# Kernel tuning notes

Hardware: AMD Instinct MI355X
Metric: run time of the kernel (lower is better)

The kernel has to match this reference:

```python
import jax, jax.numpy as jnp
import numpy as np

N = 50000
E = 800000
F = 64
HID = 64
HEADS = 4
NTYPES = 3


def layer_norm(x, g, b, eps=1e-5):
    mu = x.mean(-1, keepdims=True)
    var = ((x - mu) ** 2).mean(-1, keepdims=True)
    return (x - mu) * jax.lax.rsqrt(var + eps) * g + b


def gat_conv(x, src, dst, n, W, att_src, att_dst, bias, concat):
    # PyG GATConv: per-head linear transform, additive attention, segment softmax over dst.
    H, C = att_src.shape
    xp = (x @ W).reshape(n, H, C)                       # [N,H,C]
    a_s = (xp * att_src).sum(-1)                         # [N,H]
    a_d = (xp * att_dst).sum(-1)                         # [N,H]
    e = jax.nn.leaky_relu(a_s[src] + a_d[dst], 0.2)      # [Etot,H]
    m = jax.ops.segment_max(e, dst, num_segments=n)      # stable softmax per target
    ex = jnp.exp(e - m[dst])
    denom = jax.ops.segment_sum(ex, dst, num_segments=n)
    alpha = ex / (denom[dst] + 1e-16)                    # [Etot,H]
    msg = xp[src] * alpha[:, :, None]                    # [Etot,H,C]
    out = jax.ops.segment_sum(msg, dst, num_segments=n)  # [N,H,C]
    out = out.reshape(n, H * C) if concat else out.mean(1)
    return out + bias


def setup_inputs() -> dict:
    key = jax.random.key(0)
    ks = jax.random.split(key, 12)
    f32 = jnp.float32
    return {
        'node_features': jax.random.normal(ks[0], (N, F), f32),
        'node_types': jax.random.randint(ks[1], (N,), 0, NTYPES),
        'edge_index': jax.random.randint(ks[2], (2, E), 0, N),
        'type_emb': jax.random.normal(ks[3], (NTYPES, HID), f32) * 0.02,
        'proj_W': jax.random.normal(ks[4], (F, HID), f32) / np.sqrt(F).astype(np.float32),
        'proj_b': jnp.zeros((HID,), f32),
        'W0': jax.random.normal(ks[5], (HID, HEADS * HID), f32) / np.sqrt(HID).astype(np.float32),
        'att_src0': jax.random.normal(ks[6], (HEADS, HID), f32) * 0.1,
        'att_dst0': jax.random.normal(ks[7], (HEADS, HID), f32) * 0.1,
        'bias0': jnp.zeros((HEADS * HID,), f32),
        'ln0_g': jnp.ones((HEADS * HID,), f32),
        'ln0_b': jnp.zeros((HEADS * HID,), f32),
        'W1': jax.random.normal(ks[8], (HEADS * HID, HEADS * HID), f32) / np.sqrt(HEADS * HID).astype(np.float32),
        'att_src1': jax.random.normal(ks[9], (HEADS, HID), f32) * 0.1,
        'att_dst1': jax.random.normal(ks[10], (HEADS, HID), f32) * 0.1,
        'bias1': jnp.zeros((HID,), f32),
        'ln1_g': jnp.ones((HID,), f32),
        'ln1_b': jnp.zeros((HID,), f32),
    }


def reference(node_features, node_types, edge_index, type_emb, proj_W, proj_b,
              W0, att_src0, att_dst0, bias0, ln0_g, ln0_b,
              W1, att_src1, att_dst1, bias1, ln1_g, ln1_b):
    n = node_features.shape[0]
    loop = jnp.arange(n)
    src = jnp.concatenate([edge_index[0], loop])  # add_self_loops=True (PyG default)
    dst = jnp.concatenate([edge_index[1], loop])
    # input projection + node-type embedding
    x = node_features @ proj_W + proj_b + type_emb[node_types]
    # layer 0: concat heads -> [N, HEADS*HID]
    h = gat_conv(x, src, dst, n, W0, att_src0, att_dst0, bias0, True)
    h = jax.nn.relu(layer_norm(h, ln0_g, ln0_b))  # dropout is identity in eval
    # layer 1: mean over heads -> [N, HID]; residual skipped (shape mismatch 256 vs 64)
    h2 = gat_conv(h, src, dst, n, W1, att_src1, att_dst1, bias1, False)
    h2 = jax.nn.relu(layer_norm(h2, ln1_g, ln1_b))
    return h2
```

## Files before the change

### kernel.cpp

```cpp
#include <hip/hip_runtime.h>
#include <hip/hip_bf16.h>
#include <hip/hip_fp16.h>

typedef unsigned short u16;
typedef unsigned int u32;
typedef short s16x8 __attribute__((ext_vector_type(8)));
typedef float f32x4 __attribute__((ext_vector_type(4)));

__device__ __forceinline__ float bf2f(u16 u) {
  return __uint_as_float(((u32)u) << 16);
}

__device__ __forceinline__ u16 f2b(float f) {
  __hip_bfloat16 h = __float2bfloat16(f);
  return *(u16*)&h;
}

__device__ __forceinline__ u32 packbf(float lo, float hi) {
  return (u32)f2b(lo) | ((u32)f2b(hi) << 16);
}

__device__ __forceinline__ bool sniff_bf16(const void* ones) {
  u32 w = *(const u32*)ones;
  return (w >> 16) == (w & 0xFFFFu);
}

__device__ __forceinline__ float ldf(const void* p, size_t i, bool bf) {
  return bf ? bf2f(((const u16*)p)[i]) : ((const float*)p)[i];
}

__device__ __forceinline__ float rdlane_f(float v, int e) {
  return __uint_as_float((u32)__builtin_amdgcn_readlane((int)__float_as_uint(v), e));
}

__global__ __launch_bounds__(256) void deg_count_k(const int* __restrict__ ei, int E, int N,
                                                   int* __restrict__ deg) {
  int i = blockIdx.x * 256 + threadIdx.x;
  if (i >= E + N) return;
  int d = (i < E) ? ei[E + i] : (i - E);
  atomicAdd(deg + d, 1);
}

__global__ __launch_bounds__(256) void scan_local_k(const int* __restrict__ deg,
                                                    int* __restrict__ off,
                                                    int* __restrict__ bsum, int N) {
  __shared__ int ps[256];
  int t = threadIdx.x;
  int i = blockIdx.x * 256 + t;
  int v = (i < N) ? deg[i] : 0;
  ps[t] = v;
  __syncthreads();
#pragma unroll
  for (int o = 1; o < 256; o <<= 1) {
    int u = (t >= o) ? ps[t - o] : 0;
    __syncthreads();
    ps[t] += u;
    __syncthreads();
  }
  if (i < N) off[i] = ps[t] - v;
  if (t == 255) bsum[blockIdx.x] = ps[255];
}

__global__ __launch_bounds__(256) void scan_add2_k(int* __restrict__ off,
                                                   const int* __restrict__ bsum,
                                                   int* __restrict__ cur,
                                                   int N, int Etot, int nb) {
  __shared__ int red[256];
  int t = threadIdx.x;
  int b = blockIdx.x;
  red[t] = (t < nb && t < b) ? bsum[t] : 0;
  __syncthreads();
#pragma unroll
  for (int o = 128; o > 0; o >>= 1) {
    if (t < o) red[t] += red[t + o];
    __syncthreads();
  }
  int pre = red[0];
  int i = b * 256 + t;
  if (i == 0) off[N] = Etot;
  if (i >= N) return;
  int o2 = off[i] + pre;
  off[i] = o2;
  cur[i] = o2;
}

__global__ __launch_bounds__(256) void scatter_k(const int* __restrict__ ei, int E, int N,
                                                 int* __restrict__ cur, int* __restrict__ csr) {
  int i = blockIdx.x * 256 + threadIdx.x;
  if (i >= E + N) return;
  int s, d;
  if (i < E) { s = ei[i]; d = ei[E + i]; } else { s = i - E; d = s; }
  int p = atomicAdd(cur + d, 1);
  csr[p] = s;
}

__global__ __launch_bounds__(256) void prep_k(
    const void* __restrict__ W0, const void* __restrict__ W1,
    const void* __restrict__ pW, const void* __restrict__ atts,
    const void* __restrict__ attd, const void* __restrict__ pb,
    const void* __restrict__ temb, const void* __restrict__ ones,
    u16* __restrict__ Wp0, u16* __restrict__ Wp1, u16* __restrict__ Wpp,
    u16* __restrict__ Wpe, float* __restrict__ ca) {
  bool bf = sniff_bf16(ones);
  int b = blockIdx.x;
  int t = threadIdx.x;
  if (b < 320) {
    const void* W = (b < 64) ? W0 : W1;
    u16* Wp = (b < 64) ? Wp0 : Wp1;
    int i = (b < 64 ? b : b - 64) * 256 + t;
    int j = i & 7;
    int q = (i >> 3) & 3;
    int c = (i >> 5) & 255;
    int kc = i >> 13;
    int k = kc * 32 + q * 8 + j;
    Wp[i] = f2b(ldf(W, (size_t)k * 256 + c, bf));
  } else if (b < 336) {
    int i = (b - 320) * 256 + t;
    int j = i & 7;
    int q = (i >> 3) & 3;
    int c = (i >> 5) & 63;
    int kc = i >> 11;
    int k = kc * 32 + q * 8 + j;
    Wpp[i] = f2b(ldf(pW, (size_t)k * 64 + c, bf));
  } else {
    __shared__ float va[256], vd[256];
    int h = t >> 6, k = t & 63;
    {
      float s = 0.f, d = 0.f;
      for (int c = 0; c < 64; c++) {
        float w = ldf(W0, (size_t)k * 256 + h * 64 + c, bf);
        s += w * ldf(atts, h * 64 + c, bf);
        d += w * ldf(attd, h * 64 + c, bf);
      }
      va[t] = s;
      vd[t] = d;
    }
    __syncthreads();
    {
      int i = k;
      float wa = 0.f, wd = 0.f;
      for (int kk = 0; kk < 64; kk++) {
        float wv = ldf(pW, (size_t)i * 64 + kk, bf);
        wa += wv * va[h * 64 + kk];
        wd += wv * vd[h * 64 + kk];
      }
      int kc = i >> 5, q = (i >> 3) & 3, j = i & 7;
      Wpe[((kc * 16 + h) * 4 + q) * 8 + j] = f2b(wa);
      Wpe[((kc * 16 + 4 + h) * 4 + q) * 8 + j] = f2b(wd);
    }
    Wpe[256 + t] = 0;
    Wpe[768 + t] = 0;
    if (t < 12) {
      int ty = t >> 2, hh = t & 3;
      float sa = 0.f, sd = 0.f;
      for (int kk = 0; kk < 64; kk++) {
        float bv = ldf(pb, kk, bf) + ldf(temb, ty * 64 + kk, bf);
        sa += bv * va[hh * 64 + kk];
        sd += bv * vd[hh * 64 + kk];
      }
      ca[t] = sa;
      ca[12 + t] = sd;
    }
  }
}

__global__ __launch_bounds__(256) void proj2_k(
    const void* __restrict__ nf, const int* __restrict__ ntype,
    const u16* __restrict__ Wpp, const u16* __restrict__ Wpe,
    const void* __restrict__ pbias, const void* __restrict__ temb,
    const float* __restrict__ ca, const void* __restrict__ ones,
    u16* __restrict__ x, float* __restrict__ aS, float* __restrict__ aD, int N) {
  bool bf = sniff_bf16(ones);
  int t = threadIdx.x;
  int wave = t >> 6, lane = t & 63;
  int r = lane & 15, q = lane >> 4;
  int row0 = blockIdx.x * 16;
  int arow = row0 + r;
  if (arow >= N) arow = N - 1;
  f32x4 xacc = {0.f, 0.f, 0.f, 0.f};
  f32x4 eacc = {0.f, 0.f, 0.f, 0.f};
#pragma unroll
  for (int kc = 0; kc < 2; kc++) {
    s16x8 a;
    if (bf) {
      a = *(const s16x8*)((const u16*)nf + (size_t)arow * 64 + kc * 32 + q * 8);
    } else {
      const float* fp = (const float*)nf + (size_t)arow * 64 + kc * 32 + q * 8;
#pragma unroll
      for (int j = 0; j < 8; j++) a[j] = (short)f2b(fp[j]);
    }
    {
      int c = wave * 16 + r;
      s16x8 b = *(const s16x8*)(Wpp + (((size_t)kc * 64 + c) * 4 + q) * 8);
      xacc = __builtin_amdgcn_mfma_f32_16x16x32_bf16(a, b, xacc, 0, 0, 0);
    }
    if (wave == 3) {
      s16x8 b = *(const s16x8*)(Wpe + (((size_t)kc * 16 + r) * 4 + q) * 8);
      eacc = __builtin_amdgcn_mfma_f32_16x16x32_bf16(a, b, eacc, 0, 0, 0);
    }
  }
#pragma unroll
  for (int rg = 0; rg < 4; rg++) {
    int row = row0 + q * 4 + rg;
    if (row >= N) continue;
    int col = wave * 16 + r;
    int ty = ntype[row];
    float v = xacc[rg] + ldf(pbias, col, bf) + ldf(temb, ty * 64 + col, bf);
    x[(size_t)row * 64 + col] = f2b(v);
    if (wave == 3 && r < 8) {
      if (r < 4) aS[(size_t)row * 4 + r] = eacc[rg] + ca[ty * 4 + r];
      else       aD[(size_t)row * 4 + (r - 4)] = eacc[rg] + ca[12 + ty * 4 + (r - 4)];
    }
  }
}

__global__ __launch_bounds__(256) void agg0_k(
    const int* __restrict__ off, const int* __restrict__ csr,
    const float* __restrict__ aS, const float* __restrict__ aD,
    const u16* __restrict__ x, u16* __restrict__ Ag, int N) {
  int n = blockIdx.x * 4 + (threadIdx.x >> 6);
  int lane = threadIdx.x & 63;
  if (n >= N) return;
  int start = off[n], end = off[n + 1];
  float4 ad4 = *(const float4*)(aD + (size_t)n * 4);
  float ad[4] = {ad4.x, ad4.y, ad4.z, ad4.w};
  float den[4] = {0.f, 0.f, 0.f, 0.f};
  float acc[4] = {0.f, 0.f, 0.f, 0.f};
  const u16* xl = x + lane;

  for (int cs = start; cs < end; cs += 64) {
    int cnt = end - cs; if (cnt > 64) cnt = 64;
    int s = 0;
    float ex[4] = {0.f, 0.f, 0.f, 0.f};
    if (lane < cnt) {
      s = csr[cs + lane];
      float4 as4 = *(const float4*)(aS + (size_t)s * 4);
      float av[4] = {as4.x, as4.y, as4.z, as4.w};
#pragma unroll
      for (int h = 0; h < 4; h++) {
        float v = av[h] + ad[h];
        v = (v > 0.f ? v : 0.2f * v) - 3.0f;
        ex[h] = __expf(v);
        den[h] += ex[h];
      }
    }
#pragma unroll 8
    for (int e = 0; e < cnt; e++) {
      int se = __builtin_amdgcn_readlane(s, e);
      float w0 = rdlane_f(ex[0], e);
      float w1 = rdlane_f(ex[1], e);
      float w2 = rdlane_f(ex[2], e);
      float w3 = rdlane_f(ex[3], e);
      float xv = bf2f(xl[(size_t)se * 64]);
      acc[0] += w0 * xv;
      acc[1] += w1 * xv;
      acc[2] += w2 * xv;
      acc[3] += w3 * xv;
    }
  }
#pragma unroll
  for (int h = 0; h < 4; h++) {
#pragma unroll
    for (int o = 32; o > 0; o >>= 1) den[h] += __shfl_xor(den[h], o, 64);
    acc[h] /= (den[h] + 1e-16f);
  }
#pragma unroll
  for (int h = 0; h < 4; h++) Ag[(size_t)n * 256 + h * 64 + lane] = f2b(acc[h]);
}

__global__ __launch_bounds__(256) void l0g1_k(
    const u16* __restrict__ Ag, const u16* __restrict__ Wp0,
    const void* __restrict__ bias0, const void* __restrict__ g0,
    const void* __restrict__ be0, const u16* __restrict__ Wp1,
    const void* __restrict__ atts, const void* __restrict__ attd,
    const void* __restrict__ ones,
    u16* __restrict__ C, float* __restrict__ aS, float* __restrict__ aD, int N) {
  bool bf = sniff_bf16(ones);
  __shared__ u16 hs[16][264];
  __shared__ float sm_s[4][16], sm_q[4][16];
  int t = threadIdx.x;
  int wave = t >> 6, lane = t & 63;
  int r = lane & 15, q = lane >> 4;
  int row0 = blockIdx.x * 16;
  int arow = row0 + r;
  if (arow >= N) arow = N - 1;
  {
    const u16* ap = Ag + (size_t)arow * 256 + wave * 64 + q * 8;
    f32x4 acc[4] = {{0.f, 0.f, 0.f, 0.f}, {0.f, 0.f, 0.f, 0.f},
                    {0.f, 0.f, 0.f, 0.f}, {0.f, 0.f, 0.f, 0.f}};
#pragma unroll
    for (int kc = 0; kc < 2; kc++) {
      s16x8 a = *(const s16x8*)(ap + kc * 32);
#pragma unroll
      for (int ct = 0; ct < 4; ct++) {
        int c = wave * 64 + ct * 16 + r;
        s16x8 b = *(const s16x8*)(Wp0 + (((size_t)kc * 256 + c) * 4 + q) * 8);
        acc[ct] = __builtin_amdgcn_mfma_f32_16x16x32_bf16(a, b, acc[ct], 0, 0, 0);
      }
    }
    float yv[4][4];
    float s_p[4] = {0.f, 0.f, 0.f, 0.f};
    float q_p[4] = {0.f, 0.f, 0.f, 0.f};
#pragma unroll
    for (int ct = 0; ct < 4; ct++) {
      float bc = ldf(bias0, wave * 64 + ct * 16 + r, bf);
#pragma unroll
      for (int rg = 0; rg < 4; rg++) {
        float y = acc[ct][rg] + bc;
        yv[ct][rg] = y;
        s_p[rg] += y;
        q_p[rg] += y * y;
      }
    }
#pragma unroll
    for (int o = 1; o < 16; o <<= 1) {
#pragma unroll
      for (int rg = 0; rg < 4; rg++) {
        s_p[rg] += __shfl_xor(s_p[rg], o, 64);
        q_p[rg] += __shfl_xor(q_p[rg], o, 64);
      }
    }
    if (r == 0) {
#pragma unroll
      for (int rg = 0; rg < 4; rg++) {
        sm_s[wave][q * 4 + rg] = s_p[rg];
        sm_q[wave][q * 4 + rg] = q_p[rg];
      }
    }
    __syncthreads();
#pragma unroll
    for (int rg = 0; rg < 4; rg++) {
      int lr = q * 4 + rg;
      float mu = (sm_s[0][lr] + sm_s[1][lr] + sm_s[2][lr] + sm_s[3][lr]) * (1.f / 256.f);
      float vq = (sm_q[0][lr] + sm_q[1][lr] + sm_q[2][lr] + sm_q[3][lr]) * (1.f / 256.f) - mu * mu;
      float inv = rsqrtf(vq + 1e-5f);
#pragma unroll
      for (int ct = 0; ct < 4; ct++) {
        int c = wave * 64 + ct * 16 + r;
        float o_ = (yv[ct][rg] - mu) * inv * ldf(g0, c, bf) + ldf(be0, c, bf);
        hs[lr][c] = f2b(fmaxf(o_, 0.f));
      }
    }
  }
  __syncthreads();
  int colw = wave * 64;
  f32x4 acc[4] = {{0.f, 0.f, 0.f, 0.f}, {0.f, 0.f, 0.f, 0.f},
                  {0.f, 0.f, 0.f, 0.f}, {0.f, 0.f, 0.f, 0.f}};
#pragma unroll
  for (int kc = 0; kc < 8; kc++) {
    s16x8 a = *(const s16x8*)&hs[r][kc * 32 + q * 8];
#pragma unroll
    for (int ct = 0; ct < 4; ct++) {
      int c = colw + ct * 16 + r;
      s16x8 b = *(const s16x8*)(Wp1 + (((size_t)kc * 256 + c) * 4 + q) * 8);
      acc[ct] = __builtin_amdgcn_mfma_f32_16x16x32_bf16(a, b, acc[ct], 0, 0, 0);
    }
  }
#pragma unroll
  for (int ct = 0; ct < 4; ct++) {
#pragma unroll
    for (int rg = 0; rg < 4; rg++) {
      int row = row0 + q * 4 + rg;
      if (row < N) C[(size_t)row * 256 + colw + ct * 16 + r] = f2b(acc[ct][rg]);
    }
  }
  float sp[4] = {0.f, 0.f, 0.f, 0.f};
  float dp[4] = {0.f, 0.f, 0.f, 0.f};
#pragma unroll
  for (int ct = 0; ct < 4; ct++) {
    int c = colw + ct * 16 + r;
    float av = ldf(atts, c, bf);
    float dv = ldf(attd, c, bf);
#pragma unroll
    for (int rg = 0; rg < 4; rg++) {
      sp[rg] += acc[ct][rg] * av;
      dp[rg] += acc[ct][rg] * dv;
    }
  }
#pragma unroll
  for (int o = 1; o < 16; o <<= 1) {
#pragma unroll
    for (int rg = 0; rg < 4; rg++) {
      sp[rg] += __shfl_xor(sp[rg], o, 64);
      dp[rg] += __shfl_xor(dp[rg], o, 64);
    }
  }
  if (r == 0) {
#pragma unroll
    for (int rg = 0; rg < 4; rg++) {
      int row = row0 + q * 4 + rg;
      if (row < N) {
        aS[(size_t)row * 4 + wave] = sp[rg];
        aD[(size_t)row * 4 + wave] = dp[rg];
      }
    }
  }
}

__global__ __launch_bounds__(256) void agg1_k(
    const int* __restrict__ off, const int* __restrict__ csr,
    const float* __restrict__ aS, const float* __restrict__ aD,
    const u16* __restrict__ xp,
    const void* __restrict__ bias, const void* __restrict__ g,
    const void* __restrict__ b, void* __restrict__ out, int N) {
  bool bf = sniff_bf16(g);
  int n = blockIdx.x * 4 + (threadIdx.x >> 6);
  int lane = threadIdx.x & 63;
  if (n >= N) return;
  int start = off[n], end = off[n + 1];
  bool hiSel = (lane & 32) != 0;
  float4 ad4 = *(const float4*)(aD + (size_t)n * 4);
  float ad[4] = {ad4.x, ad4.y, ad4.z, ad4.w};
  float den[4] = {0.f, 0.f, 0.f, 0.f};
  float acc[4] = {0.f, 0.f, 0.f, 0.f};
  const u32* xp32 = (const u32*)xp;

  for (int cs = start; cs < end; cs += 64) {
    int cnt = end - cs; if (cnt > 64) cnt = 64;
    int s = 0;
    float ex[4] = {0.f, 0.f, 0.f, 0.f};
    if (lane < cnt) {
      s = csr[cs + lane];
      float4 as4 = *(const float4*)(aS + (size_t)s * 4);
      float av[4] = {as4.x, as4.y, as4.z, as4.w};
#pragma unroll
      for (int h = 0; h < 4; h++) {
        float v = av[h] + ad[h];
        v = (v > 0.f ? v : 0.2f * v) - 3.0f;
        ex[h] = __expf(v);
        den[h] += ex[h];
      }
    }
#pragma unroll 8
    for (int e = 0; e < cnt; e++) {
      int se = __builtin_amdgcn_readlane(s, e);
      float w0 = rdlane_f(ex[0], e);
      float w1 = rdlane_f(ex[1], e);
      float w2 = rdlane_f(ex[2], e);
      float w3 = rdlane_f(ex[3], e);
      float wA = hiSel ? w1 : w0;
      float wB = hiSel ? w3 : w2;
      const u32* xr = xp32 + (size_t)se * 128 + lane;
      u32 dA = xr[0];
      u32 dB = xr[64];
      acc[0] += wA * __uint_as_float(dA << 16);
      acc[1] += wA * __uint_as_float(dA & 0xffff0000u);
      acc[2] += wB * __uint_as_float(dB << 16);
      acc[3] += wB * __uint_as_float(dB & 0xffff0000u);
    }
  }
#pragma unroll
  for (int h = 0; h < 4; h++) {
#pragma unroll
    for (int o = 32; o > 0; o >>= 1) den[h] += __shfl_xor(den[h], o, 64);
  }
  {
    float dA = (hiSel ? den[1] : den[0]) + 1e-16f;
    float dB = (hiSel ? den[3] : den[2]) + 1e-16f;
    acc[0] /= dA; acc[1] /= dA;
    acc[2] /= dB; acc[3] /= dB;
  }
  float p0 = acc[0] + acc[2];
  float p1 = acc[1] + acc[3];
  p0 += __shfl_xor(p0, 32, 64);
  p1 += __shfl_xor(p1, 32, 64);
  int c = 2 * (lane & 31);
  float z0 = 0.25f * p0 + ldf(bias, c, bf);
  float z1 = 0.25f * p1 + ldf(bias, c + 1, bf);
  float sum = z0 + z1;
#pragma unroll
  for (int o = 32; o > 0; o >>= 1) sum += __shfl_xor(sum, o, 64);
  float mu = sum * (1.f / 128.f);
  float d0 = z0 - mu, d1 = z1 - mu;
  float sq = d0 * d0 + d1 * d1;
#pragma unroll
  for (int o = 32; o > 0; o >>= 1) sq += __shfl_xor(sq, o, 64);
  float inv = rsqrtf(sq * (1.f / 128.f) + 1e-5f);
  float y0 = fmaxf(d0 * inv * ldf(g, c, bf) + ldf(b, c, bf), 0.f);
  float y1 = fmaxf(d1 * inv * ldf(g, c + 1, bf) + ldf(b, c + 1, bf), 0.f);
  if (lane < 32) {
    if (bf) {
      ((u32*)out)[(size_t)n * 32 + lane] = packbf(y0, y1);
    } else {
      ((float2*)out)[(size_t)n * 32 + lane] = make_float2(y0, y1);
    }
  }
}

extern "C" void kernel_launch(void* const* d_in, const int* in_sizes, int n_in,
                              void* d_out, int out_size, void* d_ws, size_t ws_size,
                              hipStream_t stream) {
  const void* nf   = d_in[0];
  const int* ntyp  = (const int*)d_in[1];
  const int* ei    = (const int*)d_in[2];
  const void* temb = d_in[3];
  const void* pW   = d_in[4];
  const void* pb   = d_in[5];
  const void* W0   = d_in[6];
  const void* as0  = d_in[7];
  const void* ad0  = d_in[8];
  const void* b0   = d_in[9];
  const void* g0   = d_in[10];
  const void* be0  = d_in[11];
  const void* W1   = d_in[12];
  const void* as1  = d_in[13];
  const void* ad1  = d_in[14];
  const void* b1   = d_in[15];
  const void* g1   = d_in[16];
  const void* be1  = d_in[17];

  int N = in_sizes[0] / 64;
  int E = in_sizes[2] / 2;
  int Etot = E + N;

  u16* Wp0 = (u16*)d_ws;
  u16* Wp1 = Wp0 + 64 * 256;
  u16* Wpp = Wp1 + 256 * 256;
  u16* Wpe = Wpp + 64 * 64;
  u16* xb  = Wpe + 1024;
  u16* Ag  = xb + (size_t)N * 64;
  u16* A   = Ag + (size_t)N * 256;
  float* aS0b = (float*)(A + (size_t)N * 256);
  float* aD0b = aS0b + (size_t)N * 4;
  float* aS1b = aD0b + (size_t)N * 4;
  float* aD1b = aS1b + (size_t)N * 4;
  float* ca = aD1b + (size_t)N * 4;
  int* deg  = (int*)(ca + 32);
  int* off  = deg + N;
  int* csr  = off + N + 1;
  int* bsum = csr + Etot;

  dim3 b256(256);
  int nodeBlocks = (N + 3) / 4;
  int edgeBlocksT = (Etot + 255) / 256;
  int gemmBlocks = (N + 15) / 16;
  int scanBlocks = (N + 255) / 256;

  hipMemsetAsync(deg, 0, (size_t)N * sizeof(int), stream);
  deg_count_k<<<edgeBlocksT, b256, 0, stream>>>(ei, E, N, deg);
  scan_local_k<<<scanBlocks, b256, 0, stream>>>(deg, off, bsum, N);
  scan_add2_k<<<scanBlocks, b256, 0, stream>>>(off, bsum, deg, N, Etot, scanBlocks);
  scatter_k<<<edgeBlocksT, b256, 0, stream>>>(ei, E, N, deg, csr);
  prep_k<<<337, b256, 0, stream>>>(W0, W1, pW, as0, ad0, pb, temb, g0,
                                   Wp0, Wp1, Wpp, Wpe, ca);

  proj2_k<<<gemmBlocks, b256, 0, stream>>>(nf, ntyp, Wpp, Wpe, pb, temb, ca, g0,
                                           xb, aS0b, aD0b, N);
  agg0_k<<<nodeBlocks, b256, 0, stream>>>(off, csr, aS0b, aD0b, xb, Ag, N);
  l0g1_k<<<gemmBlocks, b256, 0, stream>>>(Ag, Wp0, b0, g0, be0, Wp1, as1, ad1, g0,
                                          A, aS1b, aD1b, N);
  agg1_k<<<nodeBlocks, b256, 0, stream>>>(off, csr, aS1b, aD1b, A, b1, g1, be1, d_out, N);
}
```

Measured before the change: 412.2 us.

## Stage attention weights in LDS and widen per-lane gathers in aggregation kernels

Both GAT aggregation kernels now write per-edge exp weights to a per-wave LDS buffer and read them back, instead of issuing four scalar readlanes per edge. agg0 splits the wave into two half-waves that process two edges per iteration with packed 32-bit bf16 loads. agg1 loads 64-bit chunks per lane so each 16-lane group covers one head, and reduces heads with xor shuffles before the layer norm. The aim is to cut scalar-unit pressure and raise memory-level parallelism in the gather loops, at the cost of extra LDS traffic and extra cross-lane reductions at the end.

```diff
diff --git a/kernel.cpp b/kernel.cpp
--- a/kernel.cpp
+++ b/kernel.cpp
@@ -27,10 +27,6 @@
 
 __device__ __forceinline__ float ldf(const void* p, size_t i, bool bf) {
   return bf ? bf2f(((const u16*)p)[i]) : ((const float*)p)[i];
-}
-
-__device__ __forceinline__ float rdlane_f(float v, int e) {
-  return __uint_as_float((u32)__builtin_amdgcn_readlane((int)__float_as_uint(v), e));
 }
 
 __global__ __launch_bounds__(256) void deg_count_k(const int* __restrict__ ei, int E, int N,
@@ -218,54 +214,70 @@
     const int* __restrict__ off, const int* __restrict__ csr,
     const float* __restrict__ aS, const float* __restrict__ aD,
     const u16* __restrict__ x, u16* __restrict__ Ag, int N) {
-  int n = blockIdx.x * 4 + (threadIdx.x >> 6);
+  __shared__ float wlds[4][64][4];
+  int wave = threadIdx.x >> 6;
   int lane = threadIdx.x & 63;
+  int n = blockIdx.x * 4 + wave;
   if (n >= N) return;
   int start = off[n], end = off[n + 1];
   float4 ad4 = *(const float4*)(aD + (size_t)n * 4);
   float ad[4] = {ad4.x, ad4.y, ad4.z, ad4.w};
   float den[4] = {0.f, 0.f, 0.f, 0.f};
-  float acc[4] = {0.f, 0.f, 0.f, 0.f};
-  const u16* xl = x + lane;
+  int hv = lane >> 5;
+  int cl = lane & 31;
+  float accL[4] = {0.f, 0.f, 0.f, 0.f};
+  float accH[4] = {0.f, 0.f, 0.f, 0.f};
+  const char* wbase = (const char*)&wlds[wave][0][0] + hv * 16;
+  u32 laneoff = (u32)cl * 4u;
 
   for (int cs = start; cs < end; cs += 64) {
     int cnt = end - cs; if (cnt > 64) cnt = 64;
-    int s = 0;
-    float ex[4] = {0.f, 0.f, 0.f, 0.f};
+    u32 sb = 0;
+    float ex0 = 0.f, ex1 = 0.f, ex2 = 0.f, ex3 = 0.f;
     if (lane < cnt) {
-      s = csr[cs + lane];
+      int s = csr[cs + lane];
+      sb = (u32)s << 7;
       float4 as4 = *(const float4*)(aS + (size_t)s * 4);
-      float av[4] = {as4.x, as4.y, as4.z, as4.w};
-#pragma unroll
-      for (int h = 0; h < 4; h++) {
-        float v = av[h] + ad[h];
-        v = (v > 0.f ? v : 0.2f * v) - 3.0f;
-        ex[h] = __expf(v);
-        den[h] += ex[h];
-      }
-    }
-#pragma unroll 8
-    for (int e = 0; e < cnt; e++) {
-      int se = __builtin_amdgcn_readlane(s, e);
-      float w0 = rdlane_f(ex[0], e);
-      float w1 = rdlane_f(ex[1], e);
-      float w2 = rdlane_f(ex[2], e);
-      float w3 = rdlane_f(ex[3], e);
-      float xv = bf2f(xl[(size_t)se * 64]);
-      acc[0] += w0 * xv;
-      acc[1] += w1 * xv;
-      acc[2] += w2 * xv;
-      acc[3] += w3 * xv;
+      float v0 = as4.x + ad[0]; v0 = (v0 > 0.f ? v0 : 0.2f * v0) - 3.0f; ex0 = __expf(v0);
+      float v1 = as4.y + ad[1]; v1 = (v1 > 0.f ? v1 : 0.2f * v1) - 3.0f; ex1 = __expf(v1);
+      float v2 = as4.z + ad[2]; v2 = (v2 > 0.f ? v2 : 0.2f * v2) - 3.0f; ex2 = __expf(v2);
+      float v3 = as4.w + ad[3]; v3 = (v3 > 0.f ? v3 : 0.2f * v3) - 3.0f; ex3 = __expf(v3);
+      den[0] += ex0; den[1] += ex1; den[2] += ex2; den[3] += ex3;
+    }
+    *(float4*)&wlds[wave][lane][0] = make_float4(ex0, ex1, ex2, ex3);
+#pragma unroll 4
+    for (int e = 0; e < cnt; e += 2) {
+      u32 so0 = (u32)__builtin_amdgcn_readlane((int)sb, e);
+      u32 so1 = (u32)__builtin_amdgcn_readlane((int)sb, e + 1);
+      u32 so = hv ? so1 : so0;
+      u32 d = *(const u32*)((const char*)x + (so + laneoff));
+      float4 w = *(const float4*)(wbase + e * 16);
+      float xlo = __uint_as_float(d << 16);
+      float xhi = __uint_as_float(d & 0xffff0000u);
+      accL[0] += w.x * xlo; accH[0] += w.x * xhi;
+      accL[1] += w.y * xlo; accH[1] += w.y * xhi;
+      accL[2] += w.z * xlo; accH[2] += w.z * xhi;
+      accL[3] += w.w * xlo; accH[3] += w.w * xhi;
     }
   }
 #pragma unroll
   for (int h = 0; h < 4; h++) {
 #pragma unroll
     for (int o = 32; o > 0; o >>= 1) den[h] += __shfl_xor(den[h], o, 64);
-    acc[h] /= (den[h] + 1e-16f);
-  }
-#pragma unroll
-  for (int h = 0; h < 4; h++) Ag[(size_t)n * 256 + h * 64 + lane] = f2b(acc[h]);
+  }
+#pragma unroll
+  for (int h = 0; h < 4; h++) {
+    accL[h] += __shfl_xor(accL[h], 32, 64);
+    accH[h] += __shfl_xor(accH[h], 32, 64);
+  }
+  if (lane < 32) {
+    u32* agp = (u32*)Ag + (size_t)n * 128 + lane;
+#pragma unroll
+    for (int h = 0; h < 4; h++) {
+      float inv = 1.f / (den[h] + 1e-16f);
+      agp[h * 32] = packbf(accL[h] * inv, accH[h] * inv);
+    }
+  }
 }
 
 __global__ __launch_bounds__(256) void l0g1_k(
@@ -404,49 +416,44 @@
     const void* __restrict__ bias, const void* __restrict__ g,
     const void* __restrict__ b, void* __restrict__ out, int N) {
   bool bf = sniff_bf16(g);
-  int n = blockIdx.x * 4 + (threadIdx.x >> 6);
+  __shared__ float wlds[4][64][4];
+  int wave = threadIdx.x >> 6;
   int lane = threadIdx.x & 63;
+  int n = blockIdx.x * 4 + wave;
   if (n >= N) return;
   int start = off[n], end = off[n + 1];
-  bool hiSel = (lane & 32) != 0;
   float4 ad4 = *(const float4*)(aD + (size_t)n * 4);
   float ad[4] = {ad4.x, ad4.y, ad4.z, ad4.w};
   float den[4] = {0.f, 0.f, 0.f, 0.f};
   float acc[4] = {0.f, 0.f, 0.f, 0.f};
-  const u32* xp32 = (const u32*)xp;
+  int hh = lane >> 4;
+  const float* wptr = &wlds[wave][0][0] + hh;
+  u32 laneoff = (u32)lane * 8u;
 
   for (int cs = start; cs < end; cs += 64) {
     int cnt = end - cs; if (cnt > 64) cnt = 64;
-    int s = 0;
-    float ex[4] = {0.f, 0.f, 0.f, 0.f};
+    u32 sb = 0;
+    float ex0 = 0.f, ex1 = 0.f, ex2 = 0.f, ex3 = 0.f;
     if (lane < cnt) {
-      s = csr[cs + lane];
+      int s = csr[cs + lane];
+      sb = (u32)s << 9;
       float4 as4 = *(const float4*)(aS + (size_t)s * 4);
-      float av[4] = {as4.x, as4.y, as4.z, as4.w};
-#pragma unroll
-      for (int h = 0; h < 4; h++) {
-        float v = av[h] + ad[h];
-        v = (v > 0.f ? v : 0.2f * v) - 3.0f;
-        ex[h] = __expf(v);
-        den[h] += ex[h];
-      }
-    }
+      float v0 = as4.x + ad[0]; v0 = (v0 > 0.f ? v0 : 0.2f * v0) - 3.0f; ex0 = __expf(v0);
+      float v1 = as4.y + ad[1]; v1 = (v1 > 0.f ? v1 : 0.2f * v1) - 3.0f; ex1 = __expf(v1);
+      float v2 = as4.z + ad[2]; v2 = (v2 > 0.f ? v2 : 0.2f * v2) - 3.0f; ex2 = __expf(v2);
+      float v3 = as4.w + ad[3]; v3 = (v3 > 0.f ? v3 : 0.2f * v3) - 3.0f; ex3 = __expf(v3);
+      den[0] += ex0; den[1] += ex1; den[2] += ex2; den[3] += ex3;
+    }
+    *(float4*)&wlds[wave][lane][0] = make_float4(ex0, ex1, ex2, ex3);
 #pragma unroll 8
     for (int e = 0; e < cnt; e++) {
-      int se = __builtin_amdgcn_readlane(s, e);
-      float w0 = rdlane_f(ex[0], e);
-      float w1 = rdlane_f(ex[1], e);
-      float w2 = rdlane_f(ex[2], e);
-      float w3 = rdlane_f(ex[3], e);
-      float wA = hiSel ? w1 : w0;
-      float wB = hiSel ? w3 : w2;
-      const u32* xr = xp32 + (size_t)se * 128 + lane;
-      u32 dA = xr[0];
-      u32 dB = xr[64];
-      acc[0] += wA * __uint_as_float(dA << 16);
-      acc[1] += wA * __uint_as_float(dA & 0xffff0000u);
-      acc[2] += wB * __uint_as_float(dB << 16);
-      acc[3] += wB * __uint_as_float(dB & 0xffff0000u);
+      u32 so = (u32)__builtin_amdgcn_readlane((int)sb, e);
+      uint2 d = *(const uint2*)((const char*)xp + (so + laneoff));
+      float w = wptr[e * 4];
+      acc[0] += w * __uint_as_float(d.x << 16);
+      acc[1] += w * __uint_as_float(d.x & 0xffff0000u);
+      acc[2] += w * __uint_as_float(d.y << 16);
+      acc[3] += w * __uint_as_float(d.y & 0xffff0000u);
     }
   }
 #pragma unroll
@@ -454,35 +461,38 @@
 #pragma unroll
     for (int o = 32; o > 0; o >>= 1) den[h] += __shfl_xor(den[h], o, 64);
   }
-  {
-    float dA = (hiSel ? den[1] : den[0]) + 1e-16f;
-    float dB = (hiSel ? den[3] : den[2]) + 1e-16f;
-    acc[0] /= dA; acc[1] /= dA;
-    acc[2] /= dB; acc[3] /= dB;
-  }
-  float p0 = acc[0] + acc[2];
-  float p1 = acc[1] + acc[3];
-  p0 += __shfl_xor(p0, 32, 64);
-  p1 += __shfl_xor(p1, 32, 64);
-  int c = 2 * (lane & 31);
-  float z0 = 0.25f * p0 + ldf(bias, c, bf);
-  float z1 = 0.25f * p1 + ldf(bias, c + 1, bf);
-  float sum = z0 + z1;
-#pragma unroll
-  for (int o = 32; o > 0; o >>= 1) sum += __shfl_xor(sum, o, 64);
-  float mu = sum * (1.f / 128.f);
-  float d0 = z0 - mu, d1 = z1 - mu;
-  float sq = d0 * d0 + d1 * d1;
-#pragma unroll
-  for (int o = 32; o > 0; o >>= 1) sq += __shfl_xor(sq, o, 64);
-  float inv = rsqrtf(sq * (1.f / 128.f) + 1e-5f);
-  float y0 = fmaxf(d0 * inv * ldf(g, c, bf) + ldf(b, c, bf), 0.f);
-  float y1 = fmaxf(d1 * inv * ldf(g, c + 1, bf) + ldf(b, c + 1, bf), 0.f);
-  if (lane < 32) {
+  float dsel = (hh & 2) ? ((hh & 1) ? den[3] : den[2]) : ((hh & 1) ? den[1] : den[0]);
+  float inv = 1.f / (dsel + 1e-16f);
+  float p0 = acc[0] * inv, p1 = acc[1] * inv, p2 = acc[2] * inv, p3 = acc[3] * inv;
+  p0 += __shfl_xor(p0, 16, 64); p0 += __shfl_xor(p0, 32, 64);
+  p1 += __shfl_xor(p1, 16, 64); p1 += __shfl_xor(p1, 32, 64);
+  p2 += __shfl_xor(p2, 16, 64); p2 += __shfl_xor(p2, 32, 64);
+  p3 += __shfl_xor(p3, 16, 64); p3 += __shfl_xor(p3, 32, 64);
+  int cb = (lane & 15) * 4;
+  float z0 = 0.25f * p0 + ldf(bias, cb + 0, bf);
+  float z1 = 0.25f * p1 + ldf(bias, cb + 1, bf);
+  float z2 = 0.25f * p2 + ldf(bias, cb + 2, bf);
+  float z3 = 0.25f * p3 + ldf(bias, cb + 3, bf);
+  float sum = z0 + z1 + z2 + z3;
+  sum += __shfl_xor(sum, 1, 64); sum += __shfl_xor(sum, 2, 64);
+  sum += __shfl_xor(sum, 4, 64); sum += __shfl_xor(sum, 8, 64);
+  float mu = sum * (1.f / 64.f);
+  float d0 = z0 - mu, d1 = z1 - mu, d2 = z2 - mu, d3 = z3 - mu;
+  float sq = d0 * d0 + d1 * d1 + d2 * d2 + d3 * d3;
+  sq += __shfl_xor(sq, 1, 64); sq += __shfl_xor(sq, 2, 64);
+  sq += __shfl_xor(sq, 4, 64); sq += __shfl_xor(sq, 8, 64);
+  float invs = rsqrtf(sq * (1.f / 64.f) + 1e-5f);
+  float y0 = fmaxf(d0 * invs * ldf(g, cb + 0, bf) + ldf(b, cb + 0, bf), 0.f);
+  float y1 = fmaxf(d1 * invs * ldf(g, cb + 1, bf) + ldf(b, cb + 1, bf), 0.f);
+  float y2 = fmaxf(d2 * invs * ldf(g, cb + 2, bf) + ldf(b, cb + 2, bf), 0.f);
+  float y3 = fmaxf(d3 * invs * ldf(g, cb + 3, bf) + ldf(b, cb + 3, bf), 0.f);
+  if (lane < 16) {
     if (bf) {
-      ((u32*)out)[(size_t)n * 32 + lane] = packbf(y0, y1);
+      u32* o32 = (u32*)out + (size_t)n * 32 + lane * 2;
+      o32[0] = packbf(y0, y1);
+      o32[1] = packbf(y2, y3);
     } else {
-      ((float2*)out)[(size_t)n * 32 + lane] = make_float2(y0, y1);
+      ((float4*)out)[(size_t)n * 16 + lane] = make_float4(y0, y1, y2, y3);
     }
   }
 }
```

Measured after the change: 403.4 us. 1.02x faster.
